# Performance work log

Measured on AMD Instinct MI355X. Metric: run time of the kernel, lower is better.

The kernel has to match this reference:

```python
import jax, jax.numpy as jnp
import numpy as np

B, T, H, S, L = 1, 1024, 256, 256, 4  # batch, seq_len, hidden, state(=hidden), num_layers
EPS = 1e-5


def setup_inputs() -> dict:
    key = jax.random.key(0)
    ks = jax.random.split(key, 18)
    sc = 0.02
    return {
        "x": jax.random.normal(ks[0], (B, T, H), jnp.float32),
        "W_in": jax.random.normal(ks[1], (H, H), jnp.float32) * sc,
        "b_in": jax.random.normal(ks[2], (H,), jnp.float32) * sc,
        "W1": jax.random.normal(ks[3], (L, 2 * H, H), jnp.float32) * sc,
        "b1": jax.random.normal(ks[4], (L, 2 * H), jnp.float32) * sc,
        "W2": jax.random.normal(ks[5], (L, H, 2 * H), jnp.float32) * sc,
        "b2": jax.random.normal(ks[6], (L, H), jnp.float32) * sc,
        "gamma": jnp.ones((L, H), jnp.float32),
        "beta": jnp.zeros((L, H), jnp.float32),
        "W_dt": jax.random.normal(ks[7], (H, H), jnp.float32) * sc,
        "b_dt": jax.random.normal(ks[8], (H,), jnp.float32) * sc,
        "C": jax.random.normal(ks[9], (H, S), jnp.float32) * sc,
        "D": jnp.ones((H,), jnp.float32),
        "W_out": jax.random.normal(ks[10], (H, H), jnp.float32) * sc,
        "b_out": jax.random.normal(ks[11], (H,), jnp.float32) * sc,
    }


def _layernorm(y, g, b):
    m = y.mean(-1, keepdims=True)
    v = ((y - m) ** 2).mean(-1, keepdims=True)  # biased var, as torch LayerNorm
    return (y - m) * jax.lax.rsqrt(v + EPS) * g + b


def reference(x, W_in, b_in, W1, b1, W2, b2, gamma, beta, W_dt, b_dt, C, D, W_out, b_out):
    # input projection + residual gated-MLP stack
    h = x @ W_in.T + b_in  # (B,T,H)
    for l in range(W1.shape[0]):
        y = jax.nn.gelu(h @ W1[l].T + b1[l], approximate=False) @ W2[l].T + b2[l]
        h = _layernorm(y, gamma[l], beta[l]) + h
    dt = jax.nn.sigmoid(h @ W_dt.T + b_dt)  # (B,T,H)

    # All S rows of the state are identical (state[:,0] is a broadcast of h[:,0]
    # and each row updates identically), so the recurrence collapses to an
    # H-vector scan: v_0 = h_0 ; v_i = dt_i * v_{i-1} + (1-dt_i) * h_i.
    def step(v, inp):
        dt_i, h_i = inp  # each (B,H)
        v = dt_i * v + (1.0 - dt_i) * h_i
        return v, v

    _, vs_rest = jax.lax.scan(
        step, h[:, 0], (jnp.swapaxes(dt[:, 1:], 0, 1), jnp.swapaxes(h[:, 1:], 0, 1))
    )  # (T-1,B,H)
    vs = jnp.concatenate([h[:, :1], jnp.swapaxes(vs_rest, 0, 1)], axis=1)  # (B,T,H)

    u = vs @ C.T + D * h  # (B,T,H): C @ v_i + D*h_i, identical across state rows

    hid = h.shape[-1]  # == state_size
    # Original concatenates: step 0 contributes 1 row, each step i>0 contributes
    # S (=H) identical rows -> (B, 1+(T-1)*H, H).
    rows = jnp.concatenate([u[:, :1], jnp.repeat(u[:, 1:], hid, axis=1)], axis=1)
    return rows @ W_out.T + b_out
```

## Files before the change

### kernel.cpp

```cpp
#include <hip/hip_runtime.h>
#include <hip/hip_bf16.h>


#define T_SEQ 1024
#define H_DIM 256

typedef __attribute__((ext_vector_type(8))) short short8;
typedef __attribute__((ext_vector_type(4))) float f32x4;

__device__ __forceinline__ float gelu_exact(float x) {
    return 0.5f * x * (1.0f + erff(x * 0.70710678118654752f));
}

__device__ __forceinline__ void split_bf16(float x, unsigned short& h, unsigned short& l) {
    __hip_bfloat16 bh = __float2bfloat16(x);
    float fh = __bfloat162float(bh);
    __hip_bfloat16 bl = __float2bfloat16(x - fh);
    __builtin_memcpy(&h, &bh, 2);
    __builtin_memcpy(&l, &bl, 2);
}

template<int ACT>
__global__ __launch_bounds__(256) void gemm_mfma(
    const float* __restrict__ X, const float* __restrict__ W,
    const float* __restrict__ bias, float* __restrict__ Y,
    int M, int N, int K,
    const float* __restrict__ dscale, const float* __restrict__ dmat)
{
    __shared__ unsigned short Xh[32][40], Xl[32][40], Wh[32][40], Wl[32][40];

    const int tid  = threadIdx.x;
    const int lr   = tid >> 3;
    const int lc   = (tid & 7) * 4;
    const int wave = tid >> 6;
    const int lane = tid & 63;
    const int wr   = wave >> 1, wc = wave & 1;
    const int l15  = lane & 15, ko = lane >> 4;
    const int n0   = blockIdx.x * 32;
    const int m0   = blockIdx.y * 32;

    f32x4 acc = {0.f, 0.f, 0.f, 0.f};

    for (int k0 = 0; k0 < K; k0 += 32) {
        const float4 xv = *reinterpret_cast<const float4*>(&X[(size_t)(m0 + lr) * K + k0 + lc]);
        const float4 wv = *reinterpret_cast<const float4*>(&W[(size_t)(n0 + lr) * K + k0 + lc]);
        ushort4 xh, xl, wh, wl;
        split_bf16(xv.x, xh.x, xl.x); split_bf16(xv.y, xh.y, xl.y);
        split_bf16(xv.z, xh.z, xl.z); split_bf16(xv.w, xh.w, xl.w);
        split_bf16(wv.x, wh.x, wl.x); split_bf16(wv.y, wh.y, wl.y);
        split_bf16(wv.z, wh.z, wl.z); split_bf16(wv.w, wh.w, wl.w);
        *reinterpret_cast<ushort4*>(&Xh[lr][lc]) = xh;
        *reinterpret_cast<ushort4*>(&Xl[lr][lc]) = xl;
        *reinterpret_cast<ushort4*>(&Wh[lr][lc]) = wh;
        *reinterpret_cast<ushort4*>(&Wl[lr][lc]) = wl;
        __syncthreads();

        const short8 ah = *reinterpret_cast<const short8*>(&Xh[16 * wr + l15][8 * ko]);
        const short8 al = *reinterpret_cast<const short8*>(&Xl[16 * wr + l15][8 * ko]);
        const short8 bh = *reinterpret_cast<const short8*>(&Wh[16 * wc + l15][8 * ko]);
        const short8 bl = *reinterpret_cast<const short8*>(&Wl[16 * wc + l15][8 * ko]);
        acc = __builtin_amdgcn_mfma_f32_16x16x32_bf16(ah, bh, acc, 0, 0, 0);
        acc = __builtin_amdgcn_mfma_f32_16x16x32_bf16(ah, bl, acc, 0, 0, 0);
        acc = __builtin_amdgcn_mfma_f32_16x16x32_bf16(al, bh, acc, 0, 0, 0);
        __syncthreads();
    }

    const int n_ = n0 + 16 * wc + l15;
#pragma unroll
    for (int j = 0; j < 4; ++j) {
        const int m_ = m0 + 16 * wr + 4 * ko + j;
        float r = acc[j];
        if (bias)   r += bias[n_];
        if (dscale) r += dscale[n_] * dmat[(size_t)m_ * N + n_];
        if (ACT == 1) r = gelu_exact(r);
        Y[(size_t)m_ * N + n_] = r;
    }
}

__global__ __launch_bounds__(256) void ln_residual_kernel(
    const float* __restrict__ Yin, const float* __restrict__ gamma,
    const float* __restrict__ beta, const float* __restrict__ hin,
    float* __restrict__ hout)
{
    __shared__ float red[8];
    const int row = blockIdx.x;
    const int c = threadIdx.x;
    const float y = Yin[(size_t)row * H_DIM + c];
    float s = y, s2 = y * y;
#pragma unroll
    for (int o = 1; o < 64; o <<= 1) {
        s  += __shfl_xor(s, o);
        s2 += __shfl_xor(s2, o);
    }
    const int wid = c >> 6;
    if ((c & 63) == 0) { red[wid] = s; red[4 + wid] = s2; }
    __syncthreads();
    const float ts  = red[0] + red[1] + red[2] + red[3];
    const float ts2 = red[4] + red[5] + red[6] + red[7];
    const float mean = ts * (1.0f / H_DIM);
    const float var  = ts2 * (1.0f / H_DIM) - mean * mean;
    const float inv  = rsqrtf(var + 1e-5f);
    hout[(size_t)row * H_DIM + c] =
        (y - mean) * inv * gamma[c] + beta[c] + hin[(size_t)row * H_DIM + c];
}

__global__ __launch_bounds__(1024) void scan_par(
    const float* __restrict__ dtpre, const float* __restrict__ h,
    float* __restrict__ vs)
{
    __shared__ float sA[16][64], sB[16][64];
    const int chl   = threadIdx.x & 63;
    const int chunk = threadIdx.x >> 6;
    const int c  = blockIdx.x * 64 + chl;
    const int t0 = chunk * 64;

    float A = 1.f, B = 0.f;
    for (int i = 0; i < 64; ++i) {
        const int t = t0 + i;
        const float hv = h[(size_t)t * H_DIM + c];
        float a, b;
        if (t == 0) { a = 0.f; b = hv; }
        else {
            const float dt = 1.0f / (1.0f + __expf(-dtpre[(size_t)t * H_DIM + c]));
            a = dt; b = (1.0f - dt) * hv;
        }
        A = a * A;
        B = fmaf(a, B, b);
    }
    sA[chunk][chl] = A; sB[chunk][chl] = B;
    __syncthreads();

    if (chunk == 0) {
        float pA = 1.f, pB = 0.f;
        for (int j = 0; j < 16; ++j) {
            const float cA = sA[j][chl], cB = sB[j][chl];
            sA[j][chl] = pA; sB[j][chl] = pB;
            pA = cA * pA;
            pB = fmaf(cA, pB, cB);
        }
    }
    __syncthreads();

    A = sA[chunk][chl]; B = sB[chunk][chl];
    for (int i = 0; i < 64; ++i) {
        const int t = t0 + i;
        const float hv = h[(size_t)t * H_DIM + c];
        float a, b;
        if (t == 0) { a = 0.f; b = hv; }
        else {
            const float dt = 1.0f / (1.0f + __expf(-dtpre[(size_t)t * H_DIM + c]));
            a = dt; b = (1.0f - dt) * hv;
        }
        A = a * A;
        B = fmaf(a, B, b);
        vs[(size_t)t * H_DIM + c] = B;
    }
}

__global__ __launch_bounds__(256) void replicate_f32(
    const float* __restrict__ src, float* __restrict__ out)
{
    const int i = blockIdx.x;
    const int tid = threadIdx.x;
    const int cg = tid & 63;
    const int sub = tid >> 6;

    const float4 v = *reinterpret_cast<const float4*>(&src[(size_t)i * H_DIM + cg * 4]);

    if (i == 0) {
        if (blockIdx.y == 0 && sub == 0)
            *reinterpret_cast<float4*>(&out[(size_t)cg * 4]) = v;
    } else {
        const size_t base = (size_t)(1 + (i - 1) * H_DIM + blockIdx.y * 64) * H_DIM;
#pragma unroll 4
        for (int it = 0; it < 16; ++it) {
            const size_t row_off = base + (size_t)(sub + it * 4) * H_DIM;
            *reinterpret_cast<float4*>(&out[row_off + cg * 4]) = v;
        }
    }
}

extern "C" void kernel_launch(void* const* d_in, const int* in_sizes, int n_in,
                              void* d_out, int out_size, void* d_ws, size_t ws_size,
                              hipStream_t stream)
{
    const float* x     = (const float*)d_in[0];
    const float* W_in  = (const float*)d_in[1];
    const float* b_in  = (const float*)d_in[2];
    const float* W1    = (const float*)d_in[3];
    const float* b1    = (const float*)d_in[4];
    const float* W2    = (const float*)d_in[5];
    const float* b2    = (const float*)d_in[6];
    const float* gamma = (const float*)d_in[7];
    const float* beta  = (const float*)d_in[8];
    const float* W_dt  = (const float*)d_in[9];
    const float* b_dt  = (const float*)d_in[10];
    const float* C     = (const float*)d_in[11];
    const float* D     = (const float*)d_in[12];
    const float* W_out = (const float*)d_in[13];
    const float* b_out = (const float*)d_in[14];
    float* out = (float*)d_out;

    float* ws    = (float*)d_ws;
    float* h     = ws;
    float* y1    = ws + 262144;
    float* y2    = ws + 786432;
    float* dtpre = ws + 262144;
    float* u     = ws + 524288;
    float* vs    = ws + 786432;
    float* ou    = ws + 786432;

    const dim3 blk(256);

    gemm_mfma<0><<<dim3(H_DIM / 32, T_SEQ / 32), blk, 0, stream>>>(
        x, W_in, b_in, h, T_SEQ, H_DIM, H_DIM, nullptr, nullptr);

    for (int l = 0; l < 4; ++l) {
        gemm_mfma<1><<<dim3(512 / 32, T_SEQ / 32), blk, 0, stream>>>(
            h, W1 + (size_t)l * 512 * 256, b1 + l * 512, y1,
            T_SEQ, 512, 256, nullptr, nullptr);
        gemm_mfma<0><<<dim3(H_DIM / 32, T_SEQ / 32), blk, 0, stream>>>(
            y1, W2 + (size_t)l * 256 * 512, b2 + l * 256, y2,
            T_SEQ, H_DIM, 512, nullptr, nullptr);
        ln_residual_kernel<<<dim3(T_SEQ), blk, 0, stream>>>(
            y2, gamma + l * 256, beta + l * 256, h, h);
    }

    gemm_mfma<0><<<dim3(H_DIM / 32, T_SEQ / 32), blk, 0, stream>>>(
        h, W_dt, b_dt, dtpre, T_SEQ, H_DIM, H_DIM, nullptr, nullptr);

    scan_par<<<dim3(H_DIM / 64), dim3(1024), 0, stream>>>(dtpre, h, vs);

    gemm_mfma<0><<<dim3(H_DIM / 32, T_SEQ / 32), blk, 0, stream>>>(
        vs, C, nullptr, u, T_SEQ, H_DIM, H_DIM, D, h);

    gemm_mfma<0><<<dim3(H_DIM / 32, T_SEQ / 32), blk, 0, stream>>>(
        u, W_out, b_out, ou, T_SEQ, H_DIM, H_DIM, nullptr, nullptr);

    replicate_f32<<<dim3(T_SEQ, 4), blk, 0, stream>>>(ou, out);
}
```

Baseline: 471.9 us.

## Pre-split weights to bf16 pairs, use row-block GEMMs, fuse W2 GEMM with LayerNorm

Adds a presplit kernel that converts all weight matrices to bf16 hi/lo pairs once per call, so the GEMMs no longer re-split weight tiles. The GEMMs become row-block kernels in which each block covers 32 rows across the full N, reading weights directly from global memory. The second MLP GEMM is fused with the LayerNorm and residual update through a shared-memory tile, which removes one launch and an intermediate round trip per layer. The trade-off is that the GEMM grids shrink to 32 blocks, leaving much of the GPU idle, and the weight conversion adds an extra pass over the weights on every call.

```diff
diff --git a/kernel.cpp b/kernel.cpp
--- a/kernel.cpp
+++ b/kernel.cpp
@@ -20,88 +20,201 @@
     __builtin_memcpy(&l, &bl, 2);
 }
 
-template<int ACT>
-__global__ __launch_bounds__(256) void gemm_mfma(
-    const float* __restrict__ X, const float* __restrict__ W,
-    const float* __restrict__ bias, float* __restrict__ Y,
-    int M, int N, int K,
+struct SplitArgs {
+    const float* src[6];
+    unsigned short* dh[6];
+    unsigned short* dl[6];
+    int n[6];
+};
+
+__global__ __launch_bounds__(256) void presplit_kernel(SplitArgs a) {
+    const int s = blockIdx.y;
+    const float* __restrict__ src = a.src[s];
+    unsigned short* __restrict__ dh = a.dh[s];
+    unsigned short* __restrict__ dl = a.dl[s];
+    const int n = a.n[s];
+    for (int i = blockIdx.x * 256 + threadIdx.x; i < n; i += gridDim.x * 256) {
+        unsigned short h, l;
+        split_bf16(src[i], h, l);
+        dh[i] = h; dl[i] = l;
+    }
+}
+
+template<int NTPW, int ACT>
+__global__ __launch_bounds__(256) void gemm_rb(
+    const float* __restrict__ X,
+    const unsigned short* __restrict__ Wh, const unsigned short* __restrict__ Wl,
+    const float* __restrict__ bias, float* __restrict__ Y, int K,
     const float* __restrict__ dscale, const float* __restrict__ dmat)
 {
-    __shared__ unsigned short Xh[32][40], Xl[32][40], Wh[32][40], Wl[32][40];
-
-    const int tid  = threadIdx.x;
-    const int lr   = tid >> 3;
-    const int lc   = (tid & 7) * 4;
-    const int wave = tid >> 6;
-    const int lane = tid & 63;
-    const int wr   = wave >> 1, wc = wave & 1;
-    const int l15  = lane & 15, ko = lane >> 4;
-    const int n0   = blockIdx.x * 32;
-    const int m0   = blockIdx.y * 32;
-
-    f32x4 acc = {0.f, 0.f, 0.f, 0.f};
+    const int N = NTPW * 64;
+    __shared__ unsigned short Xh[32][40], Xl[32][40];
+    const int tid = threadIdx.x;
+    const int lr = tid >> 3, lc = (tid & 7) * 4;
+    const int wave = tid >> 6, lane = tid & 63;
+    const int l15 = lane & 15, ko = lane >> 4;
+    const int m0 = blockIdx.x * 32;
+    const int ncb = wave * (NTPW * 16);
+
+    f32x4 acc[2][NTPW];
+#pragma unroll
+    for (int r = 0; r < 2; ++r)
+#pragma unroll
+        for (int c = 0; c < NTPW; ++c) acc[r][c] = (f32x4){0.f, 0.f, 0.f, 0.f};
 
     for (int k0 = 0; k0 < K; k0 += 32) {
         const float4 xv = *reinterpret_cast<const float4*>(&X[(size_t)(m0 + lr) * K + k0 + lc]);
-        const float4 wv = *reinterpret_cast<const float4*>(&W[(size_t)(n0 + lr) * K + k0 + lc]);
-        ushort4 xh, xl, wh, wl;
+        ushort4 xh, xl;
         split_bf16(xv.x, xh.x, xl.x); split_bf16(xv.y, xh.y, xl.y);
         split_bf16(xv.z, xh.z, xl.z); split_bf16(xv.w, xh.w, xl.w);
-        split_bf16(wv.x, wh.x, wl.x); split_bf16(wv.y, wh.y, wl.y);
-        split_bf16(wv.z, wh.z, wl.z); split_bf16(wv.w, wh.w, wl.w);
         *reinterpret_cast<ushort4*>(&Xh[lr][lc]) = xh;
         *reinterpret_cast<ushort4*>(&Xl[lr][lc]) = xl;
-        *reinterpret_cast<ushort4*>(&Wh[lr][lc]) = wh;
-        *reinterpret_cast<ushort4*>(&Wl[lr][lc]) = wl;
         __syncthreads();
 
-        const short8 ah = *reinterpret_cast<const short8*>(&Xh[16 * wr + l15][8 * ko]);
-        const short8 al = *reinterpret_cast<const short8*>(&Xl[16 * wr + l15][8 * ko]);
-        const short8 bh = *reinterpret_cast<const short8*>(&Wh[16 * wc + l15][8 * ko]);
-        const short8 bl = *reinterpret_cast<const short8*>(&Wl[16 * wc + l15][8 * ko]);
-        acc = __builtin_amdgcn_mfma_f32_16x16x32_bf16(ah, bh, acc, 0, 0, 0);
-        acc = __builtin_amdgcn_mfma_f32_16x16x32_bf16(ah, bl, acc, 0, 0, 0);
-        acc = __builtin_amdgcn_mfma_f32_16x16x32_bf16(al, bh, acc, 0, 0, 0);
+        short8 ah[2], al[2];
+#pragma unroll
+        for (int r = 0; r < 2; ++r) {
+            ah[r] = *reinterpret_cast<const short8*>(&Xh[16 * r + l15][8 * ko]);
+            al[r] = *reinterpret_cast<const short8*>(&Xl[16 * r + l15][8 * ko]);
+        }
+#pragma unroll
+        for (int c = 0; c < NTPW; ++c) {
+            const size_t woff = (size_t)(ncb + 16 * c + l15) * K + k0 + 8 * ko;
+            const short8 bh = *reinterpret_cast<const short8*>(&Wh[woff]);
+            const short8 bl = *reinterpret_cast<const short8*>(&Wl[woff]);
+#pragma unroll
+            for (int r = 0; r < 2; ++r) {
+                acc[r][c] = __builtin_amdgcn_mfma_f32_16x16x32_bf16(ah[r], bh, acc[r][c], 0, 0, 0);
+                acc[r][c] = __builtin_amdgcn_mfma_f32_16x16x32_bf16(ah[r], bl, acc[r][c], 0, 0, 0);
+                acc[r][c] = __builtin_amdgcn_mfma_f32_16x16x32_bf16(al[r], bh, acc[r][c], 0, 0, 0);
+            }
+        }
         __syncthreads();
     }
 
-    const int n_ = n0 + 16 * wc + l15;
-#pragma unroll
-    for (int j = 0; j < 4; ++j) {
-        const int m_ = m0 + 16 * wr + 4 * ko + j;
-        float r = acc[j];
-        if (bias)   r += bias[n_];
-        if (dscale) r += dscale[n_] * dmat[(size_t)m_ * N + n_];
-        if (ACT == 1) r = gelu_exact(r);
-        Y[(size_t)m_ * N + n_] = r;
-    }
-}
-
-__global__ __launch_bounds__(256) void ln_residual_kernel(
-    const float* __restrict__ Yin, const float* __restrict__ gamma,
-    const float* __restrict__ beta, const float* __restrict__ hin,
-    float* __restrict__ hout)
-{
-    __shared__ float red[8];
-    const int row = blockIdx.x;
-    const int c = threadIdx.x;
-    const float y = Yin[(size_t)row * H_DIM + c];
-    float s = y, s2 = y * y;
-#pragma unroll
-    for (int o = 1; o < 64; o <<= 1) {
-        s  += __shfl_xor(s, o);
-        s2 += __shfl_xor(s2, o);
-    }
-    const int wid = c >> 6;
-    if ((c & 63) == 0) { red[wid] = s; red[4 + wid] = s2; }
-    __syncthreads();
-    const float ts  = red[0] + red[1] + red[2] + red[3];
-    const float ts2 = red[4] + red[5] + red[6] + red[7];
-    const float mean = ts * (1.0f / H_DIM);
-    const float var  = ts2 * (1.0f / H_DIM) - mean * mean;
-    const float inv  = rsqrtf(var + 1e-5f);
-    hout[(size_t)row * H_DIM + c] =
-        (y - mean) * inv * gamma[c] + beta[c] + hin[(size_t)row * H_DIM + c];
+#pragma unroll
+    for (int c = 0; c < NTPW; ++c) {
+        const int n_ = ncb + 16 * c + l15;
+#pragma unroll
+        for (int r = 0; r < 2; ++r)
+#pragma unroll
+            for (int j = 0; j < 4; ++j) {
+                const int m_ = m0 + 16 * r + 4 * ko + j;
+                float v = acc[r][c][j];
+                if (bias)   v += bias[n_];
+                if (dscale) v += dscale[n_] * dmat[(size_t)m_ * N + n_];
+                if (ACT == 1) v = gelu_exact(v);
+                Y[(size_t)m_ * N + n_] = v;
+            }
+    }
+}
+
+__global__ __launch_bounds__(256) void gemm_w2_ln(
+    const float* __restrict__ Y1,
+    const unsigned short* __restrict__ Wh, const unsigned short* __restrict__ Wl,
+    const float* __restrict__ b2, const float* __restrict__ gamma,
+    const float* __restrict__ beta, float* __restrict__ h)
+{
+    const int K = 512;
+    __shared__ unsigned short Xh[32][40], Xl[32][40];
+    __shared__ float yt[32][260];
+    __shared__ float sred[32][8], s2red[32][8];
+    __shared__ float mstat[32], istat[32];
+
+    const int tid = threadIdx.x;
+    const int lr = tid >> 3, lc = (tid & 7) * 4;
+    const int wave = tid >> 6, lane = tid & 63;
+    const int l15 = lane & 15, ko = lane >> 4;
+    const int m0 = blockIdx.x * 32;
+
+    f32x4 acc[2][4];
+#pragma unroll
+    for (int r = 0; r < 2; ++r)
+#pragma unroll
+        for (int c = 0; c < 4; ++c) acc[r][c] = (f32x4){0.f, 0.f, 0.f, 0.f};
+
+    for (int k0 = 0; k0 < K; k0 += 32) {
+        const float4 xv = *reinterpret_cast<const float4*>(&Y1[(size_t)(m0 + lr) * K + k0 + lc]);
+        ushort4 xh, xl;
+        split_bf16(xv.x, xh.x, xl.x); split_bf16(xv.y, xh.y, xl.y);
+        split_bf16(xv.z, xh.z, xl.z); split_bf16(xv.w, xh.w, xl.w);
+        *reinterpret_cast<ushort4*>(&Xh[lr][lc]) = xh;
+        *reinterpret_cast<ushort4*>(&Xl[lr][lc]) = xl;
+        __syncthreads();
+
+        short8 ah[2], al[2];
+#pragma unroll
+        for (int r = 0; r < 2; ++r) {
+            ah[r] = *reinterpret_cast<const short8*>(&Xh[16 * r + l15][8 * ko]);
+            al[r] = *reinterpret_cast<const short8*>(&Xl[16 * r + l15][8 * ko]);
+        }
+#pragma unroll
+        for (int c = 0; c < 4; ++c) {
+            const size_t woff = (size_t)(wave * 64 + 16 * c + l15) * K + k0 + 8 * ko;
+            const short8 bh = *reinterpret_cast<const short8*>(&Wh[woff]);
+            const short8 bl = *reinterpret_cast<const short8*>(&Wl[woff]);
+#pragma unroll
+            for (int r = 0; r < 2; ++r) {
+                acc[r][c] = __builtin_amdgcn_mfma_f32_16x16x32_bf16(ah[r], bh, acc[r][c], 0, 0, 0);
+                acc[r][c] = __builtin_amdgcn_mfma_f32_16x16x32_bf16(ah[r], bl, acc[r][c], 0, 0, 0);
+                acc[r][c] = __builtin_amdgcn_mfma_f32_16x16x32_bf16(al[r], bh, acc[r][c], 0, 0, 0);
+            }
+        }
+        __syncthreads();
+    }
+
+#pragma unroll
+    for (int c = 0; c < 4; ++c) {
+        const int n_ = wave * 64 + 16 * c + l15;
+        const float bv = b2[n_];
+#pragma unroll
+        for (int r = 0; r < 2; ++r)
+#pragma unroll
+            for (int j = 0; j < 4; ++j)
+                yt[16 * r + 4 * ko + j][n_] = acc[r][c][j] + bv;
+    }
+    __syncthreads();
+
+    {
+        const int r = tid >> 3, g = tid & 7;
+        float s = 0.f, s2 = 0.f;
+#pragma unroll
+        for (int i = 0; i < 32; ++i) {
+            const float v = yt[r][g * 32 + i];
+            s += v; s2 += v * v;
+        }
+        sred[r][g] = s; s2red[r][g] = s2;
+    }
+    __syncthreads();
+    if (tid < 32) {
+        float s = 0.f, s2 = 0.f;
+#pragma unroll
+        for (int g = 0; g < 8; ++g) { s += sred[tid][g]; s2 += s2red[tid][g]; }
+        const float mean = s * (1.0f / H_DIM);
+        const float var  = s2 * (1.0f / H_DIM) - mean * mean;
+        mstat[tid] = mean;
+        istat[tid] = rsqrtf(var + 1e-5f);
+    }
+    __syncthreads();
+
+    {
+        const int r = tid >> 3, g = tid & 7;
+        const float mean = mstat[r], inv = istat[r];
+        const int m_ = m0 + r;
+#pragma unroll
+        for (int i0 = 0; i0 < 32; i0 += 4) {
+            const int c = g * 32 + i0;
+            const float4 hv = *reinterpret_cast<const float4*>(&h[(size_t)m_ * H_DIM + c]);
+            const float4 gv = *reinterpret_cast<const float4*>(&gamma[c]);
+            const float4 bv = *reinterpret_cast<const float4*>(&beta[c]);
+            float4 o;
+            o.x = (yt[r][c + 0] - mean) * inv * gv.x + bv.x + hv.x;
+            o.y = (yt[r][c + 1] - mean) * inv * gv.y + bv.y + hv.y;
+            o.z = (yt[r][c + 2] - mean) * inv * gv.z + bv.z + hv.z;
+            o.w = (yt[r][c + 3] - mean) * inv * gv.w + bv.w + hv.w;
+            *reinterpret_cast<float4*>(&h[(size_t)m_ * H_DIM + c]) = o;
+        }
+    }
 }
 
 __global__ __launch_bounds__(1024) void scan_par(
@@ -204,38 +317,53 @@
     float* ws    = (float*)d_ws;
     float* h     = ws;
     float* y1    = ws + 262144;
-    float* y2    = ws + 786432;
-    float* dtpre = ws + 262144;
-    float* u     = ws + 524288;
-    float* vs    = ws + 786432;
-    float* ou    = ws + 786432;
+    float* dtpre = ws + 786432;
+    float* vs    = ws + 1048576;
+    float* u     = ws + 1310720;
+    float* ou    = ws + 1572864;
+    unsigned short* wsh = (unsigned short*)(ws + 1835008);
+
+    unsigned short* Whin = wsh;               unsigned short* Wlin = wsh + 65536;
+    unsigned short* Wh1  = wsh + 131072;      unsigned short* Wl1  = wsh + 655360;
+    unsigned short* Wh2  = wsh + 1179648;     unsigned short* Wl2  = wsh + 1703936;
+    unsigned short* Whdt = wsh + 2228224;     unsigned short* Wldt = wsh + 2293760;
+    unsigned short* WhC  = wsh + 2359296;     unsigned short* WlC  = wsh + 2424832;
+    unsigned short* Whout= wsh + 2490368;     unsigned short* Wlout= wsh + 2555904;
+
+    SplitArgs sa;
+    sa.src[0] = W_in;  sa.dh[0] = Whin;  sa.dl[0] = Wlin;  sa.n[0] = 65536;
+    sa.src[1] = W1;    sa.dh[1] = Wh1;   sa.dl[1] = Wl1;   sa.n[1] = 524288;
+    sa.src[2] = W2;    sa.dh[2] = Wh2;   sa.dl[2] = Wl2;   sa.n[2] = 524288;
+    sa.src[3] = W_dt;  sa.dh[3] = Whdt;  sa.dl[3] = Wldt;  sa.n[3] = 65536;
+    sa.src[4] = C;     sa.dh[4] = WhC;   sa.dl[4] = WlC;   sa.n[4] = 65536;
+    sa.src[5] = W_out; sa.dh[5] = Whout; sa.dl[5] = Wlout; sa.n[5] = 65536;
 
     const dim3 blk(256);
 
-    gemm_mfma<0><<<dim3(H_DIM / 32, T_SEQ / 32), blk, 0, stream>>>(
-        x, W_in, b_in, h, T_SEQ, H_DIM, H_DIM, nullptr, nullptr);
+    presplit_kernel<<<dim3(256, 6), blk, 0, stream>>>(sa);
+
+    gemm_rb<4, 0><<<dim3(32), blk, 0, stream>>>(
+        x, Whin, Wlin, b_in, h, H_DIM, nullptr, nullptr);
 
     for (int l = 0; l < 4; ++l) {
-        gemm_mfma<1><<<dim3(512 / 32, T_SEQ / 32), blk, 0, stream>>>(
-            h, W1 + (size_t)l * 512 * 256, b1 + l * 512, y1,
-            T_SEQ, 512, 256, nullptr, nullptr);
-        gemm_mfma<0><<<dim3(H_DIM / 32, T_SEQ / 32), blk, 0, stream>>>(
-            y1, W2 + (size_t)l * 256 * 512, b2 + l * 256, y2,
-            T_SEQ, H_DIM, 512, nullptr, nullptr);
-        ln_residual_kernel<<<dim3(T_SEQ), blk, 0, stream>>>(
-            y2, gamma + l * 256, beta + l * 256, h, h);
-    }
-
-    gemm_mfma<0><<<dim3(H_DIM / 32, T_SEQ / 32), blk, 0, stream>>>(
-        h, W_dt, b_dt, dtpre, T_SEQ, H_DIM, H_DIM, nullptr, nullptr);
+        gemm_rb<8, 1><<<dim3(32), blk, 0, stream>>>(
+            h, Wh1 + (size_t)l * 131072, Wl1 + (size_t)l * 131072,
+            b1 + l * 512, y1, H_DIM, nullptr, nullptr);
+        gemm_w2_ln<<<dim3(32), blk, 0, stream>>>(
+            y1, Wh2 + (size_t)l * 131072, Wl2 + (size_t)l * 131072,
+            b2 + l * 256, gamma + l * 256, beta + l * 256, h);
+    }
+
+    gemm_rb<4, 0><<<dim3(32), blk, 0, stream>>>(
+        h, Whdt, Wldt, b_dt, dtpre, H_DIM, nullptr, nullptr);
 
     scan_par<<<dim3(H_DIM / 64), dim3(1024), 0, stream>>>(dtpre, h, vs);
 
-    gemm_mfma<0><<<dim3(H_DIM / 32, T_SEQ / 32), blk, 0, stream>>>(
-        vs, C, nullptr, u, T_SEQ, H_DIM, H_DIM, D, h);
-
-    gemm_mfma<0><<<dim3(H_DIM / 32, T_SEQ / 32), blk, 0, stream>>>(
-        u, W_out, b_out, ou, T_SEQ, H_DIM, H_DIM, nullptr, nullptr);
+    gemm_rb<4, 0><<<dim3(32), blk, 0, stream>>>(
+        vs, WhC, WlC, nullptr, u, H_DIM, D, h);
+
+    gemm_rb<4, 0><<<dim3(32), blk, 0, stream>>>(
+        u, Whout, Wlout, b_out, ou, H_DIM, nullptr, nullptr);
 
     replicate_f32<<<dim3(T_SEQ, 4), blk, 0, stream>>>(ou, out);
 }
```

New measurement: 692.3 us. 1.47x slower.
